# Optimization experiments

Hardware: AMD Instinct MI355X
Metric: run time of the kernel (lower is better)

Reference implementation:

```python
import jax, jax.numpy as jnp
import numpy as np

B, S, L, V = 512, 17, 81, 13030
ENC, OE, PE, H = 240, 80, 60, 200
IN = ENC + OE + PE  # 380
TEMPERATURE = 1.0


def setup_inputs() -> dict:
    key = jax.random.key(0)
    ks = jax.random.split(key, 16)
    enc = jax.random.normal(ks[0], (B, L, ENC), dtype=jnp.float32)
    in_adj_phase = jnp.zeros((B,), dtype=bool)
    loc_idxs = jax.random.randint(ks[1], (B, L), 0, S)  # which step each location decodes at
    order_masks = jax.random.bernoulli(ks[2], 0.2, (B, S, V))
    power_1h = jnp.eye(7, dtype=jnp.float32)[jax.random.randint(ks[3], (B,), 0, 7)]
    w = 0.1
    return {
        'enc': enc,
        'in_adj_phase': in_adj_phase,
        'loc_idxs': loc_idxs,
        'order_masks': order_masks,
        'power_1h': power_1h,
        'order_embedding': w * jax.random.normal(ks[4], (V, OE), dtype=jnp.float32),
        'power_W': w * jax.random.normal(ks[5], (PE, 7), dtype=jnp.float32),
        'power_b': w * jax.random.normal(ks[6], (PE,), dtype=jnp.float32),
        'W_ih': w * jax.random.normal(ks[7], (4 * H, IN), dtype=jnp.float32),
        'W_hh': w * jax.random.normal(ks[8], (4 * H, H), dtype=jnp.float32),
        'b_ih': w * jax.random.normal(ks[9], (4 * H,), dtype=jnp.float32),
        'b_hh': w * jax.random.normal(ks[10], (4 * H,), dtype=jnp.float32),
        'out_W': w * jax.random.normal(ks[11], (V, H), dtype=jnp.float32),
        'out_b': w * jax.random.normal(ks[12], (V,), dtype=jnp.float32),
        'master_alignments': jax.random.uniform(ks[13], (L, L), dtype=jnp.float32),
    }


def reference(enc, in_adj_phase, loc_idxs, order_masks, power_1h,
              order_embedding, power_W, power_b, W_ih, W_hh, b_ih, b_hh,
              out_W, out_b, master_alignments):
    # eval mode: dropout masks are not applied (self.training is False)
    power_emb = power_1h @ power_W.T + power_b  # [B, PE]
    invalid = ~jnp.any(loc_idxs != -1, axis=1)  # [B] rows with no orders to give
    keys = jax.random.split(jax.random.key(42), S)

    def step_fn(carry, xs):
        h, c, order_emb = carry
        step, mask_t, k = xs  # mask_t: [B, V]
        # alignment over locations decoded at this step
        sel = ((loc_idxs == step) | (loc_idxs == -2)).astype(enc.dtype)  # [B, L]
        align = sel @ master_alignments  # [B, L]
        denom = jnp.sum(align, axis=1, keepdims=True)
        align = jnp.where(denom != 0, align / denom, 0.0)  # NaN -> 0 as in torch
        loc_enc = jnp.einsum('bl,bld->bd', align, enc)  # [B, ENC]
        x = jnp.concatenate([loc_enc, order_emb, power_emb], axis=1)  # [B, IN]
        gates = x @ W_ih.T + b_ih + h @ W_hh.T + b_hh  # torch gate order i,f,g,o
        i, f, g, o = jnp.split(gates, 4, axis=1)
        c_new = jax.nn.sigmoid(f) * c + jax.nn.sigmoid(i) * jnp.tanh(g)
        h_new = jax.nn.sigmoid(o) * jnp.tanh(c_new)
        scores = h_new @ out_W.T + out_b  # [B, V]
        m = jnp.where(invalid[:, None], True, mask_t)
        scores = jnp.minimum(scores, m.astype(scores.dtype) * 1e9 - 1e8)
        idx = jax.random.categorical(k, scores / TEMPERATURE, axis=-1)  # [B]
        order_emb_new = order_embedding[idx]  # [B, OE]
        return (h_new, c_new, order_emb_new), (idx, scores)

    carry0 = (jnp.zeros((B, H), enc.dtype), jnp.zeros((B, H), enc.dtype),
              jnp.zeros((B, OE), enc.dtype))
    xs = (jnp.arange(S), jnp.transpose(order_masks, (1, 0, 2)), keys)
    _, (idxs, scores) = jax.lax.scan(step_fn, carry0, xs)
    return jnp.transpose(idxs, (1, 0)), jnp.transpose(scores, (1, 0, 2))
```

## Files before the change

kernel.cpp:

```cpp
#include <hip/hip_runtime.h>
#include <math.h>

#define NB 512
#define NS 17
#define NL 81
#define NV 13030
#define NENC 240
#define NOE 80
#define NPE 60
#define NH 200
#define NIN 380
#define NG 800
#define KP 224
#define KG 608
#define NVP 13056
#define NGP 832
#define NBLK 204

#define XH_ENC 224
#define XH_OE  464
#define XH_PE  544

typedef short bf8_t __attribute__((ext_vector_type(8)));
typedef float f4_t __attribute__((ext_vector_type(4)));

__device__ __forceinline__ unsigned short f2bf(float f) {
  unsigned u = __float_as_uint(f);
  unsigned r = (u + 0x7fffu + ((u >> 16) & 1u)) >> 16;
  return (unsigned short)r;
}

__device__ __host__ __forceinline__ unsigned rotl32h(unsigned x, int d) {
  return (x << d) | (x >> (32 - d));
}
__device__ __host__ __forceinline__ void threefry2x32(
    unsigned k0, unsigned k1, unsigned x0, unsigned x1,
    unsigned& y0, unsigned& y1) {
  unsigned ks2 = k0 ^ k1 ^ 0x1BD11BDAu;
  x0 += k0; x1 += k1;
#define TFR(r) { x0 += x1; x1 = rotl32h(x1, r); x1 ^= x0; }
  TFR(13) TFR(15) TFR(26) TFR(6)
  x0 += k1;  x1 += ks2 + 1u;
  TFR(17) TFR(29) TFR(16) TFR(24)
  x0 += ks2; x1 += k0 + 2u;
  TFR(13) TFR(15) TFR(26) TFR(6)
  x0 += k0;  x1 += k1 + 3u;
  TFR(17) TFR(29) TFR(16) TFR(24)
  x0 += k1;  x1 += ks2 + 4u;
  TFR(13) TFR(15) TFR(26) TFR(6)
  x0 += ks2; x1 += k0 + 5u;
#undef TFR
  y0 = x0; y1 = x1;
}

__device__ __forceinline__ float gumbel_from_bits(unsigned bits) {
  float u = __uint_as_float((bits >> 9) | 0x3f800000u) - 1.0f;
  if (u == 0.0f) u = 1.17549435e-38f;
  return -__logf(-__logf(u));
}

__global__ void __launch_bounds__(256) prep_wcat_kernel(
    const float* __restrict__ W_ih, const float* __restrict__ W_hh,
    unsigned short* __restrict__ Wcat) {
  int t = blockIdx.x * 256 + threadIdx.x;
  if (t >= NGP * KG) return;
  int n = t / KG, k = t % KG;
  float v = 0.f;
  if (n < NG) {
    if (k < NH) v = W_hh[n * NH + k];
    else if (k >= XH_ENC && k < XH_PE + NPE) v = W_ih[n * NIN + (k - XH_ENC)];
  }
  Wcat[t] = f2bf(v);
}

__global__ void __launch_bounds__(256) prep_outw_kernel(
    const float* __restrict__ out_W, unsigned short* __restrict__ outWb) {
  int t = blockIdx.x * 256 + threadIdx.x;
  if (t >= NVP * KP) return;
  int n = t / KP, k = t % KP;
  outWb[t] = f2bf((n < NV && k < NH) ? out_W[n * NH + k] : 0.f);
}

__global__ void __launch_bounds__(256) misc_kernel(
    const float* __restrict__ power_1h, const float* __restrict__ power_W,
    const float* __restrict__ power_b, const int* __restrict__ loc_idxs,
    const float* __restrict__ b_ih, const float* __restrict__ b_hh,
    unsigned short* __restrict__ xh, float* __restrict__ bcat,
    int* __restrict__ invalid) {
  int t = blockIdx.x * 256 + threadIdx.x;
  if (t < NB * NPE) {
    int b = t / NPE, p = t % NPE;
    float a = power_b[p];
#pragma unroll
    for (int k = 0; k < 7; ++k) a = fmaf(power_1h[b * 7 + k], power_W[p * 7 + k], a);
    xh[(size_t)b * KG + XH_PE + p] = f2bf(a);
  }
  if (t < NG) bcat[t] = b_ih[t] + b_hh[t];
  if (t < NB) {
    bool any = false;
    for (int l = 0; l < NL; ++l) any = any || (loc_idxs[t * NL + l] != -1);
    invalid[t] = any ? 0 : 1;
  }
}

__global__ void __launch_bounds__(256) locenc_kernel(
    const int* __restrict__ loc_idxs, const float* __restrict__ MA,
    const float* __restrict__ enc, unsigned short* __restrict__ locenc,
    unsigned short* __restrict__ xh) {
  const int b = blockIdx.x, tid = threadIdx.x;
  __shared__ float sMA[NL * NL];
  __shared__ float sAln[NS][NL];
  __shared__ float sDen[NS];
  __shared__ int sLi[NL];
  if (tid < NL) sLi[tid] = loc_idxs[b * NL + tid];
  for (int e = tid; e < NL * NL; e += 256) sMA[e] = MA[e];
  __syncthreads();
  for (int e = tid; e < NS * NL; e += 256) {
    int s = e / NL, j = e % NL;
    float a = 0.f;
    for (int l = 0; l < NL; ++l) {
      float sel = (sLi[l] == s || sLi[l] == -2) ? 1.0f : 0.0f;
      a = fmaf(sel, sMA[l * NL + j], a);
    }
    sAln[s][j] = a;
  }
  __syncthreads();
  if (tid < NS) {
    float d = 0.f;
    for (int l = 0; l < NL; ++l) d += sAln[tid][l];
    sDen[tid] = d;
  }
  __syncthreads();
  for (int e = tid; e < NS * NL; e += 256) {
    int s = e / NL, j = e % NL;
    sAln[s][j] = (sDen[s] != 0.f) ? sAln[s][j] / sDen[s] : 0.f;
  }
  __syncthreads();
  if (tid < NENC) {
    float acc[NS];
#pragma unroll
    for (int s = 0; s < NS; ++s) acc[s] = 0.f;
    const float* eb = enc + (size_t)b * NL * NENC + tid;
    for (int l = 0; l < NL; ++l) {
      float e = eb[(size_t)l * NENC];
#pragma unroll
      for (int s = 0; s < NS; ++s) acc[s] = fmaf(sAln[s][l], e, acc[s]);
    }
#pragma unroll
    for (int s = 0; s < NS; ++s) {
      unsigned short v = f2bf(acc[s]);
      locenc[((size_t)s * NB + b) * NENC + tid] = v;
      if (s == 0) xh[(size_t)b * KG + XH_ENC + tid] = v;
    }
  }
}

__global__ void __launch_bounds__(256) build_x_kernel(
    const int* __restrict__ loc_idxs, const float* __restrict__ MA,
    const float* __restrict__ enc, unsigned short* __restrict__ xh, int step) {
  __shared__ float sel[NL];
  __shared__ float aln[NL];
  __shared__ float denom;
  const int b = blockIdx.x, tid = threadIdx.x;
  if (tid < NL) {
    int li = loc_idxs[b * NL + tid];
    sel[tid] = (li == step || li == -2) ? 1.0f : 0.0f;
  }
  __syncthreads();
  if (tid < NL) {
    float a = 0.f;
    for (int l = 0; l < NL; ++l) a = fmaf(sel[l], MA[l * NL + tid], a);
    aln[tid] = a;
  }
  __syncthreads();
  if (tid == 0) {
    float d = 0.f;
    for (int l = 0; l < NL; ++l) d += aln[l];
    denom = d;
  }
  __syncthreads();
  if (tid < NL) aln[tid] = (denom != 0.f) ? aln[tid] / denom : 0.0f;
  __syncthreads();
  if (tid < NENC) {
    const float* eb = enc + (size_t)b * NL * NENC + tid;
    float a = 0.f;
    for (int l = 0; l < NL; ++l) a = fmaf(aln[l], eb[(size_t)l * NENC], a);
    xh[(size_t)b * KG + XH_ENC + tid] = f2bf(a);
  }
}

__device__ __forceinline__ void mfma_nt_16x64(
    const unsigned short* __restrict__ A, const unsigned short* __restrict__ B,
    int lda, int ldb, int m0w, int n0, int nk, f4_t acc[4]) {
  const int lane = threadIdx.x & 63;
  const int tx = lane & 15, quad = lane >> 4;
  const unsigned short* ap = A + (size_t)(m0w + tx) * lda + quad * 8;
  const unsigned short* bp0 = B + (size_t)(n0 + tx) * ldb + quad * 8;
  for (int kc = 0; kc < nk; ++kc) {
    bf8_t a = *(const bf8_t*)(ap + kc * 32);
#pragma unroll
    for (int jf = 0; jf < 4; ++jf) {
      bf8_t b = *(const bf8_t*)(bp0 + (size_t)jf * 16 * ldb + kc * 32);
      acc[jf] = __builtin_amdgcn_mfma_f32_16x16x32_bf16(a, b, acc[jf], 0, 0, 0);
    }
  }
}

__global__ void __launch_bounds__(256) gates_kernel(
    const unsigned short* __restrict__ xh, const unsigned short* __restrict__ Wcat,
    const float* __restrict__ bcat, float* __restrict__ gates) {
  const int w = threadIdx.x >> 6;
  const int lane = threadIdx.x & 63;
  const int tx = lane & 15, quad = lane >> 4;
  const int m0w = blockIdx.y * 64 + w * 16;
  const int n0 = blockIdx.x * 64;
  f4_t acc[4] = {};
  mfma_nt_16x64(xh, Wcat, KG, KG, m0w, n0, KG / 32, acc);
#pragma unroll
  for (int jf = 0; jf < 4; ++jf) {
    int n = n0 + jf * 16 + tx;
    if (n >= NG) continue;
    float bias = bcat[n];
#pragma unroll
    for (int reg = 0; reg < 4; ++reg) {
      int m = m0w + quad * 4 + reg;
      gates[(size_t)m * NG + n] = acc[jf][reg] + bias;
    }
  }
}

__global__ void __launch_bounds__(256) lstm_cell_kernel(
    const float* __restrict__ gates, unsigned short* __restrict__ xh,
    float* __restrict__ c) {
  int t = blockIdx.x * 256 + threadIdx.x;
  if (t >= NB * NH) return;
  int b = t / NH, j = t % NH;
  const float* g = gates + (size_t)b * NG;
  float gi = g[j], gf = g[NH + j], gg = g[2 * NH + j], go = g[3 * NH + j];
  float si = 1.f / (1.f + expf(-gi));
  float sf = 1.f / (1.f + expf(-gf));
  float so = 1.f / (1.f + expf(-go));
  float cn = sf * c[t] + si * tanhf(gg);
  float hn = so * tanhf(cn);
  c[t] = cn;
  xh[(size_t)b * KG + j] = f2bf(hn);
}

__global__ void __launch_bounds__(256) scores_kernel(
    const unsigned short* __restrict__ xh, const unsigned short* __restrict__ outWb,
    const float* __restrict__ out_b, const int* __restrict__ order_masks,
    const int* __restrict__ invalid, float* __restrict__ out,
    float* __restrict__ pval, int* __restrict__ pidx,
    int step, unsigned k0, unsigned k1) {
  const int w = threadIdx.x >> 6;
  const int lane = threadIdx.x & 63;
  const int tx = lane & 15, quad = lane >> 4;
  const int m0w = blockIdx.y * 64 + w * 16;
  const int n0 = blockIdx.x * 64;
  f4_t acc[4] = {};
  mfma_nt_16x64(xh, outWb, KG, KP, m0w, n0, KP / 32, acc);

  float bias[4];
  int nn[4];
#pragma unroll
  for (int jf = 0; jf < 4; ++jf) {
    nn[jf] = n0 + jf * 16 + tx;
    bias[jf] = (nn[jf] < NV) ? out_b[nn[jf]] : 0.f;
  }

  float bval[4];
  int bidx[4];
#pragma unroll
  for (int reg = 0; reg < 4; ++reg) {
    const int m = m0w + quad * 4 + reg;
    const int inv = invalid[m];
    const int* mrow = order_masks + (size_t)m * NS * NV + (size_t)step * NV;
    float* orow = out + (size_t)NB * NS + ((size_t)m * NS + step) * (size_t)NV;
    float vals[4];
#pragma unroll
    for (int jf = 0; jf < 4; ++jf) {
      int n = nn[jf];
      float v = -1.0e8f;
      if (n < NV) {
        int msk = inv ? 1 : mrow[n];
        v = fminf(acc[jf][reg] + bias[jf], msk ? 9.0e8f : -1.0e8f);
        orow[n] = v;
      }
      vals[jf] = v;
    }
    unsigned base = (unsigned)m * (unsigned)NV;
    unsigned y0, y1, y2, y3;
    threefry2x32(k0, k1, base + (unsigned)nn[0], base + (unsigned)nn[1], y0, y1);
    threefry2x32(k0, k1, base + (unsigned)nn[2], base + (unsigned)nn[3], y2, y3);
    float g[4] = {gumbel_from_bits(y0), gumbel_from_bits(y1),
                  gumbel_from_bits(y2), gumbel_from_bits(y3)};
    float bv = -INFINITY; int bi = 0;
#pragma unroll
    for (int jf = 0; jf < 4; ++jf) {
      float cnd = (nn[jf] < NV) ? vals[jf] + g[jf] : -INFINITY;
      if (cnd > bv) { bv = cnd; bi = nn[jf]; }
    }
    bval[reg] = bv; bidx[reg] = bi;
  }
#pragma unroll
  for (int s = 8; s >= 1; s >>= 1) {
#pragma unroll
    for (int reg = 0; reg < 4; ++reg) {
      float ov = __shfl_xor(bval[reg], s);
      int oi = __shfl_xor(bidx[reg], s);
      if (ov > bval[reg]) { bval[reg] = ov; bidx[reg] = oi; }
    }
  }
#pragma unroll
  for (int reg = 0; reg < 4; ++reg) {
    if (tx == reg) {
      int m = m0w + quad * 4 + reg;
      pval[(size_t)m * NBLK + blockIdx.x] = bval[reg];
      pidx[(size_t)m * NBLK + blockIdx.x] = bidx[reg];
    }
  }
}

__global__ void __launch_bounds__(256) sample_kernel(
    const float* __restrict__ pval, const int* __restrict__ pidx,
    const float* __restrict__ order_embedding,
    const unsigned short* __restrict__ locenc,
    unsigned short* __restrict__ xh, float* __restrict__ out, int step) {
  const int m = blockIdx.x, tid = threadIdx.x;
  __shared__ float sv[256];
  __shared__ int si[256];
  float v = -INFINITY; int i = 0;
  if (tid < NBLK) { v = pval[(size_t)m * NBLK + tid]; i = pidx[(size_t)m * NBLK + tid]; }
  sv[tid] = v; si[tid] = i;
  __syncthreads();
  for (int off = 128; off > 0; off >>= 1) {
    if (tid < off) {
      float v2 = sv[tid + off]; int i2 = si[tid + off];
      if (v2 > sv[tid] || (v2 == sv[tid] && i2 < si[tid])) { sv[tid] = v2; si[tid] = i2; }
    }
    __syncthreads();
  }
  if (tid == 0) out[m * NS + step] = (float)si[0];
  if (tid < NOE) {
    int idx = si[0];
    xh[(size_t)m * KG + XH_OE + tid] = f2bf(order_embedding[(size_t)idx * NOE + tid]);
  }
  if (locenc != nullptr && step + 1 < NS && tid < NENC) {
    xh[(size_t)m * KG + XH_ENC + tid] =
        locenc[((size_t)(step + 1) * NB + m) * NENC + tid];
  }
}

extern "C" void kernel_launch(void* const* d_in, const int* in_sizes, int n_in,
                              void* d_out, int out_size, void* d_ws, size_t ws_size,
                              hipStream_t stream) {
  const float* enc          = (const float*)d_in[0];
  const int*   loc_idxs     = (const int*)d_in[2];
  const int*   order_masks  = (const int*)d_in[3];
  const float* power_1h     = (const float*)d_in[4];
  const float* order_embedding = (const float*)d_in[5];
  const float* power_W      = (const float*)d_in[6];
  const float* power_b      = (const float*)d_in[7];
  const float* W_ih         = (const float*)d_in[8];
  const float* W_hh         = (const float*)d_in[9];
  const float* b_ih         = (const float*)d_in[10];
  const float* b_hh         = (const float*)d_in[11];
  const float* out_W        = (const float*)d_in[12];
  const float* out_b        = (const float*)d_in[13];
  const float* MA           = (const float*)d_in[14];

  float* ws      = (float*)d_ws;
  float* c       = ws;
  float* gates   = c + NB * NH;
  float* pval    = gates + NB * NG;
  float* bcat    = pval + NB * NBLK;
  int*   pidx    = (int*)(bcat + NG);
  int*   invalid = pidx + NB * NBLK;
  unsigned short* xh     = (unsigned short*)(invalid + NB);
  unsigned short* Wcat   = xh + (size_t)NB * KG;
  unsigned short* outWb  = Wcat + (size_t)NGP * KG;
  unsigned short* locenc = outWb + (size_t)NVP * KP;

  const size_t base_bytes =
      (size_t)(NB * NH + NB * NG + NB * NBLK + NG) * 4 +
      (size_t)(NB * NBLK + NB) * 4 +
      ((size_t)NB * KG + (size_t)NGP * KG + (size_t)NVP * KP) * 2;
  const size_t locenc_bytes = (size_t)NS * NB * NENC * 2;
  const bool use_locenc = (ws_size >= base_bytes + locenc_bytes);
  if (!use_locenc) locenc = nullptr;

  float* out = (float*)d_out;

  hipMemsetAsync(xh, 0, sizeof(unsigned short) * (size_t)NB * KG, stream);
  hipMemsetAsync(c, 0, sizeof(float) * (size_t)NB * NH, stream);
  misc_kernel<<<(NB * NPE + 255) / 256, 256, 0, stream>>>(
      power_1h, power_W, power_b, loc_idxs, b_ih, b_hh, xh, bcat, invalid);
  prep_wcat_kernel<<<(NGP * KG + 255) / 256, 256, 0, stream>>>(W_ih, W_hh, Wcat);
  prep_outw_kernel<<<(NVP * KP + 255) / 256, 256, 0, stream>>>(out_W, outWb);
  if (use_locenc) {
    locenc_kernel<<<NB, 256, 0, stream>>>(loc_idxs, MA, enc, locenc, xh);
  }

  unsigned key[2 * NS];
  for (unsigned i = 0; i < NS; ++i) {
    unsigned y0, y1;
    threefry2x32(0u, 42u, i, i + NS, y0, y1);
    key[2 * i] = y0;
    threefry2x32(0u, 42u, i, i + NS, y0, y1);
    key[2 * i + 1] = y1;
  }

  dim3 gGates(NGP / 64, NB / 64);
  dim3 gScores(NBLK, NB / 64);
  for (int s = 0; s < NS; ++s) {
    if (!use_locenc) {
      build_x_kernel<<<NB, 256, 0, stream>>>(loc_idxs, MA, enc, xh, s);
    }
    gates_kernel<<<gGates, 256, 0, stream>>>(xh, Wcat, bcat, gates);
    lstm_cell_kernel<<<(NB * NH + 255) / 256, 256, 0, stream>>>(gates, xh, c);
    scores_kernel<<<gScores, 256, 0, stream>>>(
        xh, outWb, out_b, order_masks, invalid, out, pval, pidx,
        s, key[2 * s], key[2 * s + 1]);
    sample_kernel<<<NB, 256, 0, stream>>>(
        pval, pidx, order_embedding, locenc, xh, out, s);
  }
}
```

Baseline: 1.836 ms.

## Replace per-step sample kernel with atomicMax argmax and fuse gathers into neighbours

Each scores block now folds its per-row best value and index into a packed 64-bit key and does an atomicMax per row. This removes the partial-result buffers and the separate sample reduction kernel. The order-embedding gather and output write for the previous step move into the gates kernel prologue, and the next step's loc-enc copy moves into the LSTM cell kernel, which also resets the atomic keys. A final small kernel writes the last step's index. The aim is to cut one launch per step and the partial-result round trip, at the cost of redundant embedding gathers across gate column blocks and global atomics.

```diff
diff --git a/kernel.cpp b/kernel.cpp
--- a/kernel.cpp
+++ b/kernel.cpp
@@ -28,6 +28,12 @@
   unsigned u = __float_as_uint(f);
   unsigned r = (u + 0x7fffu + ((u >> 16) & 1u)) >> 16;
   return (unsigned short)r;
+}
+
+__device__ __forceinline__ unsigned long long enc_key(float v, int idx) {
+  unsigned b = __float_as_uint(v);
+  b = (b & 0x80000000u) ? ~b : (b | 0x80000000u);
+  return ((unsigned long long)b << 32) | (unsigned)(~(unsigned)idx);
 }
 
 __device__ __host__ __forceinline__ unsigned rotl32h(unsigned x, int d) {
@@ -207,15 +213,38 @@
 }
 
 __global__ void __launch_bounds__(256) gates_kernel(
-    const unsigned short* __restrict__ xh, const unsigned short* __restrict__ Wcat,
-    const float* __restrict__ bcat, float* __restrict__ gates) {
-  const int w = threadIdx.x >> 6;
-  const int lane = threadIdx.x & 63;
+    const unsigned short* __restrict__ xh_c, unsigned short* __restrict__ xh,
+    const unsigned short* __restrict__ Wcat, const float* __restrict__ bcat,
+    const unsigned long long* __restrict__ amax,
+    const float* __restrict__ order_embedding,
+    float* __restrict__ gates, float* __restrict__ out, int step) {
+  const int tid = threadIdx.x;
+  const int m0 = blockIdx.y * 64;
+  __shared__ int sIdx[64];
+
+  if (step > 0) {
+    if (tid < 64) {
+      unsigned long long k = amax[m0 + tid];
+      int idx = (int)(~(unsigned)k);
+      sIdx[tid] = idx;
+      if (blockIdx.x == 0) out[(size_t)(m0 + tid) * NS + (step - 1)] = (float)idx;
+    }
+    __syncthreads();
+    for (int e = tid; e < 64 * NOE; e += 256) {
+      int rr = e / NOE, col = e % NOE;
+      xh[(size_t)(m0 + rr) * KG + XH_OE + col] =
+          f2bf(order_embedding[(size_t)sIdx[rr] * NOE + col]);
+    }
+    __syncthreads();
+  }
+
+  const int w = tid >> 6;
+  const int lane = tid & 63;
   const int tx = lane & 15, quad = lane >> 4;
-  const int m0w = blockIdx.y * 64 + w * 16;
+  const int m0w = m0 + w * 16;
   const int n0 = blockIdx.x * 64;
   f4_t acc[4] = {};
-  mfma_nt_16x64(xh, Wcat, KG, KG, m0w, n0, KG / 32, acc);
+  mfma_nt_16x64(xh_c, Wcat, KG, KG, m0w, n0, KG / 32, acc);
 #pragma unroll
   for (int jf = 0; jf < 4; ++jf) {
     int n = n0 + jf * 16 + tx;
@@ -231,26 +260,34 @@
 
 __global__ void __launch_bounds__(256) lstm_cell_kernel(
     const float* __restrict__ gates, unsigned short* __restrict__ xh,
-    float* __restrict__ c) {
+    float* __restrict__ c, unsigned long long* __restrict__ amax,
+    const unsigned short* __restrict__ locenc, int step) {
   int t = blockIdx.x * 256 + threadIdx.x;
-  if (t >= NB * NH) return;
-  int b = t / NH, j = t % NH;
-  const float* g = gates + (size_t)b * NG;
-  float gi = g[j], gf = g[NH + j], gg = g[2 * NH + j], go = g[3 * NH + j];
-  float si = 1.f / (1.f + expf(-gi));
-  float sf = 1.f / (1.f + expf(-gf));
-  float so = 1.f / (1.f + expf(-go));
-  float cn = sf * c[t] + si * tanhf(gg);
-  float hn = so * tanhf(cn);
-  c[t] = cn;
-  xh[(size_t)b * KG + j] = f2bf(hn);
+  if (t < NB * NH) {
+    int b = t / NH, j = t % NH;
+    const float* g = gates + (size_t)b * NG;
+    float gi = g[j], gf = g[NH + j], gg = g[2 * NH + j], go = g[3 * NH + j];
+    float si = 1.f / (1.f + expf(-gi));
+    float sf = 1.f / (1.f + expf(-gf));
+    float so = 1.f / (1.f + expf(-go));
+    float cn = sf * c[t] + si * tanhf(gg);
+    float hn = so * tanhf(cn);
+    c[t] = cn;
+    xh[(size_t)b * KG + j] = f2bf(hn);
+  }
+  if (t < NB) amax[t] = 0ull;
+  if (locenc != nullptr && step + 1 < NS && t < NB * NENC) {
+    int b = t / NENC, col = t % NENC;
+    xh[(size_t)b * KG + XH_ENC + col] =
+        locenc[((size_t)(step + 1) * NB + b) * NENC + col];
+  }
 }
 
 __global__ void __launch_bounds__(256) scores_kernel(
     const unsigned short* __restrict__ xh, const unsigned short* __restrict__ outWb,
     const float* __restrict__ out_b, const int* __restrict__ order_masks,
     const int* __restrict__ invalid, float* __restrict__ out,
-    float* __restrict__ pval, int* __restrict__ pidx,
+    unsigned long long* __restrict__ amax,
     int step, unsigned k0, unsigned k1) {
   const int w = threadIdx.x >> 6;
   const int lane = threadIdx.x & 63;
@@ -315,39 +352,17 @@
   for (int reg = 0; reg < 4; ++reg) {
     if (tx == reg) {
       int m = m0w + quad * 4 + reg;
-      pval[(size_t)m * NBLK + blockIdx.x] = bval[reg];
-      pidx[(size_t)m * NBLK + blockIdx.x] = bidx[reg];
-    }
-  }
-}
-
-__global__ void __launch_bounds__(256) sample_kernel(
-    const float* __restrict__ pval, const int* __restrict__ pidx,
-    const float* __restrict__ order_embedding,
-    const unsigned short* __restrict__ locenc,
-    unsigned short* __restrict__ xh, float* __restrict__ out, int step) {
-  const int m = blockIdx.x, tid = threadIdx.x;
-  __shared__ float sv[256];
-  __shared__ int si[256];
-  float v = -INFINITY; int i = 0;
-  if (tid < NBLK) { v = pval[(size_t)m * NBLK + tid]; i = pidx[(size_t)m * NBLK + tid]; }
-  sv[tid] = v; si[tid] = i;
-  __syncthreads();
-  for (int off = 128; off > 0; off >>= 1) {
-    if (tid < off) {
-      float v2 = sv[tid + off]; int i2 = si[tid + off];
-      if (v2 > sv[tid] || (v2 == sv[tid] && i2 < si[tid])) { sv[tid] = v2; si[tid] = i2; }
-    }
-    __syncthreads();
-  }
-  if (tid == 0) out[m * NS + step] = (float)si[0];
-  if (tid < NOE) {
-    int idx = si[0];
-    xh[(size_t)m * KG + XH_OE + tid] = f2bf(order_embedding[(size_t)idx * NOE + tid]);
-  }
-  if (locenc != nullptr && step + 1 < NS && tid < NENC) {
-    xh[(size_t)m * KG + XH_ENC + tid] =
-        locenc[((size_t)(step + 1) * NB + m) * NENC + tid];
+      atomicMax(&amax[m], enc_key(bval[reg], bidx[reg]));
+    }
+  }
+}
+
+__global__ void __launch_bounds__(256) final_sample_kernel(
+    const unsigned long long* __restrict__ amax, float* __restrict__ out) {
+  int t = blockIdx.x * 256 + threadIdx.x;
+  if (t < NB) {
+    unsigned long long k = amax[t];
+    out[(size_t)t * NS + (NS - 1)] = (float)(int)(~(unsigned)k);
   }
 }
 
@@ -380,6 +395,8 @@
   unsigned short* Wcat   = xh + (size_t)NB * KG;
   unsigned short* outWb  = Wcat + (size_t)NGP * KG;
   unsigned short* locenc = outWb + (size_t)NVP * KP;
+  unsigned long long* amax = (unsigned long long*)pval;
+  (void)pidx;
 
   const size_t base_bytes =
       (size_t)(NB * NH + NB * NG + NB * NBLK + NG) * 4 +
@@ -412,16 +429,18 @@
 
   dim3 gGates(NGP / 64, NB / 64);
   dim3 gScores(NBLK, NB / 64);
+  const int lstm_blocks = (NB * NENC + 255) / 256;
   for (int s = 0; s < NS; ++s) {
     if (!use_locenc) {
       build_x_kernel<<<NB, 256, 0, stream>>>(loc_idxs, MA, enc, xh, s);
     }
-    gates_kernel<<<gGates, 256, 0, stream>>>(xh, Wcat, bcat, gates);
-    lstm_cell_kernel<<<(NB * NH + 255) / 256, 256, 0, stream>>>(gates, xh, c);
+    gates_kernel<<<gGates, 256, 0, stream>>>(
+        xh, xh, Wcat, bcat, amax, order_embedding, gates, out, s);
+    lstm_cell_kernel<<<lstm_blocks, 256, 0, stream>>>(
+        gates, xh, c, amax, locenc, s);
     scores_kernel<<<gScores, 256, 0, stream>>>(
-        xh, outWb, out_b, order_masks, invalid, out, pval, pidx,
+        xh, outWb, out_b, order_masks, invalid, out, amax,
         s, key[2 * s], key[2 * s + 1]);
-    sample_kernel<<<NB, 256, 0, stream>>>(
-        pval, pidx, order_embedding, locenc, xh, out, s);
-  }
-}
+  }
+  final_sample_kernel<<<(NB + 255) / 256, 256, 0, stream>>>(amax, out);
+}
```

Measured after the change: 1.858 ms. Within noise of the previous version (+1.2%).
